# Optimization experiments

Hardware: AMD Instinct MI355X
Metric: run time of the kernel (lower is better)

## Reference

```python
import jax, jax.numpy as jnp
import numpy as np

H, C = 8, 32          # heads, channels per head; H*C = 256 triggers the LN branch
N_NODES = 30000       # nodes per node type
N_EDGES = 100000      # edges per edge type
N_TYPES = 6           # hardwired edge types (all src = Package_Name)
D_IN = 128            # raw input feature dim (Package_Name stays at 128)
LRELU_SLOPE = 0.2     # PyG GATConv default negative_slope


def _segment_softmax(e, dst, n):
    # softmax of per-edge logits e [E,H] grouped by destination node
    m = jax.ops.segment_max(e, dst, num_segments=n)
    ex = jnp.exp(e - m[dst])
    den = jax.ops.segment_sum(ex, dst, num_segments=n)
    return ex / (den[dst] + 1e-16)


def _gat(x_src, x_tgt, src, dst, Ws, Wd, a_s, a_d, b):
    # bipartite GATConv, concat heads, no self loops, no edge features
    hs = (x_src @ Ws).reshape(-1, H, C)   # [Ns,H,C]
    hd = (x_tgt @ Wd).reshape(-1, H, C)   # [Nt,H,C]
    es = jnp.einsum('nhc,hc->nh', hs, a_s)
    ed = jnp.einsum('nhc,hc->nh', hd, a_d)
    e = jax.nn.leaky_relu(es[src] + ed[dst], negative_slope=LRELU_SLOPE)  # [E,H]
    n = x_tgt.shape[0]
    alpha = _segment_softmax(e, dst, n)                                   # [E,H]
    msg = hs[src] * alpha[:, :, None]                                     # [E,H,C]
    out = jax.ops.segment_sum(msg, dst, num_segments=n).reshape(n, H * C) + b
    return out, alpha


def _ln_relu(x, g, b):
    mu = x.mean(-1, keepdims=True)
    var = ((x - mu) ** 2).mean(-1, keepdims=True)
    return jax.nn.relu((x - mu) / jnp.sqrt(var + 1e-5) * g + b)


def setup_inputs() -> dict:
    key = jax.random.key(0)
    ks = jax.random.split(key, 16)
    s = 0.05
    return {
        'x_pkg': jax.random.normal(ks[0], (N_NODES, D_IN), jnp.float32),
        'x_tgt': jax.random.normal(ks[1], (N_TYPES, N_NODES, D_IN), jnp.float32),
        'edge_index': jax.random.randint(ks[2], (N_TYPES, 2, N_EDGES), 0, N_NODES, jnp.int32),
        'W1_src': jax.random.normal(ks[3], (N_TYPES, D_IN, H * C), jnp.float32) * s,
        'W1_dst': jax.random.normal(ks[4], (N_TYPES, D_IN, H * C), jnp.float32) * s,
        'att1_src': jax.random.normal(ks[5], (N_TYPES, H, C), jnp.float32) * s,
        'att1_dst': jax.random.normal(ks[6], (N_TYPES, H, C), jnp.float32) * s,
        'b1': jnp.zeros((N_TYPES, H * C), jnp.float32),
        'W2_src': jax.random.normal(ks[7], (N_TYPES, D_IN, H * C), jnp.float32) * s,
        'W2_dst': jax.random.normal(ks[8], (N_TYPES, H * C, H * C), jnp.float32) * s,
        'att2_src': jax.random.normal(ks[9], (N_TYPES, H, C), jnp.float32) * s,
        'att2_dst': jax.random.normal(ks[10], (N_TYPES, H, C), jnp.float32) * s,
        'b2': jnp.zeros((N_TYPES, H * C), jnp.float32),
        'gamma': jnp.ones((N_TYPES, H * C), jnp.float32),
        'beta': jnp.zeros((N_TYPES, H * C), jnp.float32),
        'Wc': jax.random.normal(ks[11], (N_TYPES * H * C + D_IN, 1), jnp.float32) * s,
        'bc': jnp.zeros((1,), jnp.float32),
    }


def reference(x_pkg, x_tgt, edge_index, W1_src, W1_dst, att1_src, att1_dst, b1,
              W2_src, W2_dst, att2_src, att2_dst, b2, gamma, beta, Wc, bc):
    def layer(xt, ei, Ws, Wd, a_s, a_d, bb):
        return _gat(x_pkg, xt, ei[0], ei[1], Ws, Wd, a_s, a_d, bb)

    vlayer = jax.vmap(layer, in_axes=(0, 0, 0, 0, 0, 0, 0))

    # layer 1: Package_Name -> each of 6 target types; Package_Name itself unchanged
    out1, _ = vlayer(x_tgt, edge_index, W1_src, W1_dst, att1_src, att1_dst, b1)
    x1 = jax.vmap(_ln_relu)(out1, gamma, beta)   # module reuses ln1 after both layers

    # layer 2: src features are still the raw 128-d Package_Name features
    out2, alpha2 = vlayer(x1, edge_index, W2_src, W2_dst, att2_src, att2_dst, b2)
    x2 = jax.vmap(_ln_relu)(out2, gamma, beta)

    # global mean pool per node type, concat (6 targets then Package_Name), classify
    pooled = jnp.concatenate([x2.mean(axis=1).reshape(-1), x_pkg.mean(axis=0)])
    logits = pooled @ Wc[:, 0] + bc[0]
    return logits, alpha2
```

## Files before the change

kernel.cpp:

```cpp
#include <hip/hip_runtime.h>
#include <hip/hip_bf16.h>
#include <cstddef>

#define N_NODES 30000
#define N_EDGES 100000
#define N_TYPES 6
#define D_IN 128
#define HC 256
#define NH 8
#define CH 32

typedef __attribute__((ext_vector_type(8))) unsigned short ushort8_t;
typedef __attribute__((ext_vector_type(4))) unsigned short ushort4_t;
typedef __attribute__((ext_vector_type(8))) __bf16 bf16x8;
typedef __attribute__((ext_vector_type(4))) float floatx4;

#define L2_NPB 32
#define L2_GRID ((N_NODES + L2_NPB - 1) / L2_NPB)

__device__ inline unsigned short f2bf(float f) {
    unsigned u = __float_as_uint(f);
    u += 0x7fffu + ((u >> 16) & 1u);
    return (unsigned short)(u >> 16);
}
__device__ inline float bf2f(unsigned short u) {
    return __uint_as_float(((unsigned)u) << 16);
}

__global__ void zero4(float4* __restrict__ p, int n4) {
    int g = blockIdx.x * blockDim.x + threadIdx.x;
    if (g < n4) p[g] = make_float4(0.f, 0.f, 0.f, 0.f);
}
__global__ void zero_i(int* __restrict__ p, int n) {
    int g = blockIdx.x * blockDim.x + threadIdx.x;
    if (g < n) p[g] = 0;
}
__global__ void to_bf16(const float* __restrict__ x, unsigned short* __restrict__ o, int n4) {
    int g = blockIdx.x * blockDim.x + threadIdx.x;
    if (g >= n4) return;
    float4 v = ((const float4*)x)[g];
    ushort4_t p;
    p[0] = f2bf(v.x); p[1] = f2bf(v.y); p[2] = f2bf(v.z); p[3] = f2bf(v.w);
    *(ushort4_t*)&o[(size_t)g * 4] = p;
}

__global__ void hist_all(const int* __restrict__ ei, int* __restrict__ counts) {
    int t = blockIdx.y;
    int e = blockIdx.x * 256 + threadIdx.x;
    if (e < N_EDGES)
        atomicAdd(&counts[t * N_NODES + ei[(size_t)t * 2 * N_EDGES + N_EDGES + e]], 1);
}

#define SCAN_T 1024
#define SCAN_C 30
__global__ __launch_bounds__(1024) void scan_all(const int* __restrict__ counts_g,
                                                 int* __restrict__ row_ptr_g,
                                                 int* __restrict__ cursor_g) {
    int t = blockIdx.x;
    const int* counts = counts_g + t * N_NODES;
    int* row_ptr = row_ptr_g + t * (N_NODES + 1);
    int* cursor = cursor_g + t * N_NODES;
    __shared__ int part[SCAN_T];
    int tid = threadIdx.x;
    int base = tid * SCAN_C;
    int loc[SCAN_C];
    int s = 0;
    #pragma unroll
    for (int i = 0; i < SCAN_C; ++i) {
        int idx = base + i;
        int v = (idx < N_NODES) ? counts[idx] : 0;
        loc[i] = s; s += v;
    }
    part[tid] = s;
    __syncthreads();
    int tot = s;
    for (int d = 1; d < SCAN_T; d <<= 1) {
        int v = (tid >= d) ? part[tid - d] : 0;
        __syncthreads();
        part[tid] += v;
        __syncthreads();
    }
    int off = part[tid] - tot;
    #pragma unroll
    for (int i = 0; i < SCAN_C; ++i) {
        int idx = base + i;
        if (idx < N_NODES) { int r = off + loc[i]; row_ptr[idx] = r; cursor[idx] = r; }
    }
    if (tid == SCAN_T - 1) row_ptr[N_NODES] = part[SCAN_T - 1];
}

__global__ void fill_all(const int* __restrict__ ei, int* __restrict__ cursor,
                         int* __restrict__ elist) {
    int t = blockIdx.y;
    int e = blockIdx.x * 256 + threadIdx.x;
    if (e < N_EDGES) {
        const int* src = ei + (size_t)t * 2 * N_EDGES;
        const int* dst = src + N_EDGES;
        int pos = atomicAdd(&cursor[t * N_NODES + dst[e]], 1);
        elist[t * N_EDGES + pos] = src[e];
    }
}

__global__ void att_weight_all(const float* __restrict__ W1d, const float* __restrict__ a1d,
                               const float* __restrict__ W2d, const float* __restrict__ a2d,
                               float* __restrict__ wd1, float* __restrict__ wd2) {
    int g = blockIdx.x * blockDim.x + threadIdx.x;
    const int per_t = (D_IN + HC) * NH;
    if (g >= N_TYPES * per_t) return;
    int t = g / per_t, r = g % per_t;
    if (r < D_IN * NH) {
        int k = r >> 3, h = r & 7;
        const float* wr = W1d + (size_t)t * D_IN * HC + (size_t)k * HC + h * CH;
        const float* ar = a1d + t * HC + h * CH;
        float s = 0.f;
        #pragma unroll
        for (int c = 0; c < CH; ++c) s += wr[c] * ar[c];
        wd1[t * D_IN * NH + r] = s;
    } else {
        r -= D_IN * NH;
        int k = r >> 3, h = r & 7;
        const float* wr = W2d + (size_t)t * HC * HC + (size_t)k * HC + h * CH;
        const float* ar = a2d + t * HC + h * CH;
        float s = 0.f;
        #pragma unroll
        for (int c = 0; c < CH; ++c) s += wr[c] * ar[c];
        wd2[t * HC * NH + r] = s;
    }
}

__global__ __launch_bounds__(256) void gemm_all(const unsigned short* __restrict__ A,
                                                const float* __restrict__ W1s,
                                                const float* __restrict__ W2s,
                                                const float* __restrict__ att1,
                                                const float* __restrict__ att2,
                                                unsigned short* __restrict__ hs_all,
                                                float* __restrict__ es_all) {
    const int j = blockIdx.z;
    const float* B = (j < 6) ? W1s + (size_t)j * D_IN * HC
                             : W2s + (size_t)(j - 6) * D_IN * HC;
    const float* att = (j < 6) ? att1 + j * HC : att2 + (j - 6) * HC;
    unsigned short* Cp = hs_all + (size_t)j * N_NODES * HC;
    float* e_out = es_all + (size_t)j * N_NODES * NH;

    __shared__ unsigned short As[64 * 40];
    __shared__ unsigned short Bs[64 * 40];

    const int tid = threadIdx.x;
    const int w = tid >> 6;
    const int lane = tid & 63;
    const int col = lane & 15;
    const int quad = lane >> 4;
    const int m0 = blockIdx.x * 64;
    const int n0 = blockIdx.y * 64;

    const int am = tid >> 2;
    const int ak = (tid & 3) * 8;
    const int bk2 = (tid >> 4) * 2;
    const int bn4 = (tid & 15) * 4;

    floatx4 acc[4];
    #pragma unroll
    for (int ct = 0; ct < 4; ++ct) acc[ct] = (floatx4){0.f, 0.f, 0.f, 0.f};

    #pragma unroll
    for (int k0 = 0; k0 < D_IN; k0 += 32) {
        {
            int gm = m0 + am;
            ushort8_t v = (ushort8_t){0, 0, 0, 0, 0, 0, 0, 0};
            if (gm < N_NODES) v = *(const ushort8_t*)&A[(size_t)gm * D_IN + k0 + ak];
            *(ushort8_t*)&As[am * 40 + ak] = v;
        }
        {
            const float4 r0 = *(const float4*)&B[(size_t)(k0 + bk2) * HC + n0 + bn4];
            const float4 r1 = *(const float4*)&B[(size_t)(k0 + bk2 + 1) * HC + n0 + bn4];
            float a0[4] = {r0.x, r0.y, r0.z, r0.w};
            float a1[4] = {r1.x, r1.y, r1.z, r1.w};
            #pragma unroll
            for (int q = 0; q < 4; ++q) {
                unsigned pk = (unsigned)f2bf(a0[q]) | ((unsigned)f2bf(a1[q]) << 16);
                *(unsigned*)&Bs[(bn4 + q) * 40 + bk2] = pk;
            }
        }
        __syncthreads();
        {
            ushort8_t araw = *(const ushort8_t*)&As[(w * 16 + col) * 40 + quad * 8];
            bf16x8 af = __builtin_bit_cast(bf16x8, araw);
            #pragma unroll
            for (int ct = 0; ct < 4; ++ct) {
                ushort8_t braw = *(const ushort8_t*)&Bs[(ct * 16 + col) * 40 + quad * 8];
                bf16x8 bf = __builtin_bit_cast(bf16x8, braw);
                acc[ct] = __builtin_amdgcn_mfma_f32_16x16x32_bf16(af, bf, acc[ct], 0, 0, 0);
            }
        }
        __syncthreads();
    }

    #pragma unroll
    for (int ct = 0; ct < 4; ++ct) {
        #pragma unroll
        for (int r = 0; r < 4; ++r) {
            int gm = m0 + w * 16 + quad * 4 + r;
            if (gm < N_NODES) Cp[(size_t)gm * HC + n0 + ct * 16 + col] = f2bf(acc[ct][r]);
        }
    }

    float attv[4];
    #pragma unroll
    for (int ct = 0; ct < 4; ++ct) attv[ct] = att[n0 + ct * 16 + col];
    const int hbase = n0 >> 5;
    #pragma unroll
    for (int r = 0; r < 4; ++r) {
        float h0v = acc[0][r] * attv[0] + acc[1][r] * attv[1];
        float h1v = acc[2][r] * attv[2] + acc[3][r] * attv[3];
        #pragma unroll
        for (int off = 1; off < 16; off <<= 1) {
            h0v += __shfl_xor(h0v, off);
            h1v += __shfl_xor(h1v, off);
        }
        if (col == 0) {
            int gm = m0 + w * 16 + quad * 4 + r;
            if (gm < N_NODES) {
                e_out[gm * NH + hbase] = h0v;
                e_out[gm * NH + hbase + 1] = h1v;
            }
        }
    }
}

__global__ __launch_bounds__(256) void gather_l1_all(const int* __restrict__ row_ptr_g,
                                                     const int* __restrict__ elist_g,
                                                     const float* __restrict__ es_all,
                                                     const float* __restrict__ x_tgt,
                                                     const float* __restrict__ wd1,
                                                     const unsigned short* __restrict__ hs_all,
                                                     const float* __restrict__ b1,
                                                     const float* __restrict__ gamma,
                                                     const float* __restrict__ beta,
                                                     const float* __restrict__ wd2,
                                                     float* __restrict__ ed2g_all) {
    const int t = blockIdx.y;
    const int* row_ptr = row_ptr_g + t * (N_NODES + 1);
    const int* elist = elist_g + t * N_EDGES;
    const float* es = es_all + (size_t)t * N_NODES * NH;
    const float* xd = x_tgt + (size_t)t * N_NODES * D_IN;
    const float* w1 = wd1 + t * D_IN * NH;
    const unsigned short* hs = hs_all + (size_t)t * N_NODES * HC;
    const float* bias = b1 + t * HC;
    const float* gam = gamma + t * HC;
    const float* bet = beta + t * HC;
    const float* w2 = wd2 + t * HC * NH;
    float* ed2g = ed2g_all + (size_t)t * N_NODES * NH;

    const int lane = threadIdx.x & 63;
    const int d = blockIdx.x * 4 + (threadIdx.x >> 6);

    float e1v[8];
    #pragma unroll
    for (int h = 0; h < 8; ++h) e1v[h] = 0.f;
    #pragma unroll
    for (int rep = 0; rep < 2; ++rep) {
        int k = rep * 64 + lane;
        float xv = xd[(size_t)d * D_IN + k];
        const float* wr = w1 + k * 8;
        #pragma unroll
        for (int h = 0; h < 8; ++h) e1v[h] += xv * wr[h];
    }
    #pragma unroll
    for (int off = 1; off < 64; off <<= 1)
        #pragma unroll
        for (int h = 0; h < 8; ++h) e1v[h] += __shfl_xor(e1v[h], off);

    const int h_l = lane >> 3;
    const float ed_mine = e1v[h_l];
    const int e0 = row_ptr[d], e1n = row_ptr[d + 1];

    float den = 0.f;
    float4 acc = make_float4(0.f, 0.f, 0.f, 0.f);
    for (int i = e0; i < e1n; ++i) {
        int s = elist[i];
        float x = es[s * NH + h_l] + ed_mine;
        x = (x >= 0.f) ? x : 0.2f * x;
        float ex = __expf(x);
        den += ex;
        ushort4_t hv = *(const ushort4_t*)&hs[(size_t)s * HC + lane * 4];
        acc.x += ex * bf2f(hv[0]); acc.y += ex * bf2f(hv[1]);
        acc.z += ex * bf2f(hv[2]); acc.w += ex * bf2f(hv[3]);
    }
    float inv = 1.f / (den + 1e-16f);
    float4 bv = *(const float4*)&bias[lane * 4];
    acc.x = acc.x * inv + bv.x; acc.y = acc.y * inv + bv.y;
    acc.z = acc.z * inv + bv.z; acc.w = acc.w * inv + bv.w;

    float s1 = acc.x + acc.y + acc.z + acc.w;
    float s2 = acc.x * acc.x + acc.y * acc.y + acc.z * acc.z + acc.w * acc.w;
    #pragma unroll
    for (int off = 1; off < 64; off <<= 1) { s1 += __shfl_xor(s1, off); s2 += __shfl_xor(s2, off); }
    float mu = s1 * (1.f / 256.f);
    float var = s2 * (1.f / 256.f) - mu * mu;
    float rstd = rsqrtf(var + 1e-5f);
    float4 g4 = *(const float4*)&gam[lane * 4];
    float4 b4 = *(const float4*)&bet[lane * 4];
    float ya[4];
    ya[0] = fmaxf((acc.x - mu) * rstd * g4.x + b4.x, 0.f);
    ya[1] = fmaxf((acc.y - mu) * rstd * g4.y + b4.y, 0.f);
    ya[2] = fmaxf((acc.z - mu) * rstd * g4.z + b4.z, 0.f);
    ya[3] = fmaxf((acc.w - mu) * rstd * g4.w + b4.w, 0.f);

    float e2v[8];
    #pragma unroll
    for (int h = 0; h < 8; ++h) e2v[h] = 0.f;
    #pragma unroll
    for (int q = 0; q < 4; ++q) {
        int c = lane * 4 + q;
        const float* wr = w2 + c * 8;
        #pragma unroll
        for (int h = 0; h < 8; ++h) e2v[h] += ya[q] * wr[h];
    }
    #pragma unroll
    for (int off = 1; off < 64; off <<= 1)
        #pragma unroll
        for (int h = 0; h < 8; ++h) e2v[h] += __shfl_xor(e2v[h], off);
    if (lane < 8) ed2g[d * NH + lane] = e2v[lane];
}

__global__ __launch_bounds__(256) void gather_l2_all(const int* __restrict__ row_ptr_g,
                                                     const int* __restrict__ elist_g,
                                                     const float* __restrict__ es_all,
                                                     const float* __restrict__ ed2g_all,
                                                     const unsigned short* __restrict__ hs_all,
                                                     const float* __restrict__ b2,
                                                     const float* __restrict__ gamma,
                                                     const float* __restrict__ beta,
                                                     float* __restrict__ deng_all,
                                                     float* __restrict__ ppart) {
    const int t = blockIdx.y;
    const int* row_ptr = row_ptr_g + t * (N_NODES + 1);
    const int* elist = elist_g + t * N_EDGES;
    const float* es = es_all + (size_t)(6 + t) * N_NODES * NH;
    const float* ed2g = ed2g_all + (size_t)t * N_NODES * NH;
    const unsigned short* hs = hs_all + (size_t)(6 + t) * N_NODES * HC;
    const float* bias = b2 + t * HC;
    const float* gam = gamma + t * HC;
    const float* bet = beta + t * HC;
    float* deng = deng_all + (size_t)t * N_NODES * NH;
    float* psum_part = ppart + (size_t)t * L2_GRID * HC;

    const int tid = threadIdx.x;
    const int lane = tid & 63;
    const int w = tid >> 6;
    const int h_l = lane >> 3;
    const float4 bv = *(const float4*)&bias[lane * 4];
    const float4 g4 = *(const float4*)&gam[lane * 4];
    const float4 b4 = *(const float4*)&bet[lane * 4];

    float4 pool = make_float4(0.f, 0.f, 0.f, 0.f);
    const int base = blockIdx.x * L2_NPB;

    #pragma unroll 1
    for (int rep = 0; rep < L2_NPB / 4; ++rep) {
        const int d = base + rep * 4 + w;
        if (d >= N_NODES) break;

        const float ed_mine = ed2g[d * NH + h_l];
        const int e0 = row_ptr[d], e1n = row_ptr[d + 1];

        float den = 0.f;
        float4 acc = make_float4(0.f, 0.f, 0.f, 0.f);
        for (int i = e0; i < e1n; ++i) {
            int s = elist[i];
            float x = es[s * NH + h_l] + ed_mine;
            x = (x >= 0.f) ? x : 0.2f * x;
            float ex = __expf(x);
            den += ex;
            ushort4_t hv = *(const ushort4_t*)&hs[(size_t)s * HC + lane * 4];
            acc.x += ex * bf2f(hv[0]); acc.y += ex * bf2f(hv[1]);
            acc.z += ex * bf2f(hv[2]); acc.w += ex * bf2f(hv[3]);
        }
        if ((lane & 7) == 0) deng[d * NH + h_l] = den;
        float inv = 1.f / (den + 1e-16f);
        acc.x = acc.x * inv + bv.x; acc.y = acc.y * inv + bv.y;
        acc.z = acc.z * inv + bv.z; acc.w = acc.w * inv + bv.w;

        float s1 = acc.x + acc.y + acc.z + acc.w;
        float s2 = acc.x * acc.x + acc.y * acc.y + acc.z * acc.z + acc.w * acc.w;
        #pragma unroll
        for (int off = 1; off < 64; off <<= 1) { s1 += __shfl_xor(s1, off); s2 += __shfl_xor(s2, off); }
        float mu = s1 * (1.f / 256.f);
        float var = s2 * (1.f / 256.f) - mu * mu;
        float rstd = rsqrtf(var + 1e-5f);
        pool.x += fmaxf((acc.x - mu) * rstd * g4.x + b4.x, 0.f);
        pool.y += fmaxf((acc.y - mu) * rstd * g4.y + b4.y, 0.f);
        pool.z += fmaxf((acc.z - mu) * rstd * g4.z + b4.z, 0.f);
        pool.w += fmaxf((acc.w - mu) * rstd * g4.w + b4.w, 0.f);
    }

    __shared__ float sacc[4][260];
    *(float4*)&sacc[w][lane * 4] = pool;
    __syncthreads();
    float tot = sacc[0][tid] + sacc[1][tid] + sacc[2][tid] + sacc[3][tid];
    psum_part[(size_t)blockIdx.x * HC + tid] = tot;
}

__global__ __launch_bounds__(256) void pool_reduce_all(const float* __restrict__ ppart,
                                                       float* __restrict__ psums) {
    int t = blockIdx.y;
    const float* part = ppart + (size_t)t * L2_GRID * HC;
    int tid = threadIdx.x;
    float acc = 0.f;
    for (int b = blockIdx.x; b < L2_GRID; b += gridDim.x)
        acc += part[(size_t)b * HC + tid];
    atomicAdd(&psums[t * HC + tid], acc);
}

__global__ void alpha_all(const int* __restrict__ ei,
                          const float* __restrict__ es_all,
                          const float* __restrict__ ed2g_all,
                          const float* __restrict__ deng_all,
                          float* __restrict__ out) {
    int t = blockIdx.y;
    int g = blockIdx.x * 256 + threadIdx.x;
    if (g >= N_EDGES * NH) return;
    int e = g >> 3, h = g & 7;
    const int* src = ei + (size_t)t * 2 * N_EDGES;
    const int* dst = src + N_EDGES;
    int s = src[e], d = dst[e];
    const float* es = es_all + (size_t)(6 + t) * N_NODES * NH;
    float x = es[s * NH + h] + ed2g_all[(size_t)t * N_NODES * NH + d * NH + h];
    x = (x >= 0.f) ? x : 0.2f * x;
    out[(size_t)t * N_EDGES * NH + g] =
        __expf(x) / (deng_all[(size_t)t * N_NODES * NH + d * NH + h] + 1e-16f);
}

__global__ __launch_bounds__(256) void pkg_accum(const float* __restrict__ x, float* __restrict__ sums) {
    int tid = threadIdx.x;
    int col = tid & 127;
    int rof = tid >> 7;
    float acc = 0.f;
    for (int r = blockIdx.x * 2 + rof; r < N_NODES; r += gridDim.x * 2)
        acc += x[(size_t)r * D_IN + col];
    atomicAdd(&sums[col], acc);
}

__global__ __launch_bounds__(256) void logits_k(const float* __restrict__ psums,
                                                const float* __restrict__ ksums,
                                                const float* __restrict__ Wc,
                                                const float* __restrict__ bc,
                                                float* __restrict__ out) {
    int tid = threadIdx.x;
    const float inv = 1.f / (float)N_NODES;
    float acc = 0.f;
    for (int i = tid; i < N_TYPES * HC; i += 256) acc += psums[i] * inv * Wc[i];
    if (tid < D_IN) acc += ksums[tid] * inv * Wc[N_TYPES * HC + tid];
    #pragma unroll
    for (int off = 32; off; off >>= 1) acc += __shfl_down(acc, off);
    __shared__ float w[4];
    if ((tid & 63) == 0) w[tid >> 6] = acc;
    __syncthreads();
    if (tid == 0) out[0] = w[0] + w[1] + w[2] + w[3] + bc[0];
}

static inline void zf(float* p, int n, hipStream_t stream) {
    int n4 = (n + 3) >> 2;
    zero4<<<(n4 + 255) / 256, 256, 0, stream>>>((float4*)p, n4);
}

extern "C" void kernel_launch(void* const* d_in, const int* in_sizes, int n_in,
                              void* d_out, int out_size, void* d_ws, size_t ws_size,
                              hipStream_t stream) {
    const float* x_pkg    = (const float*)d_in[0];
    const float* x_tgt    = (const float*)d_in[1];
    const int*   ei       = (const int*)d_in[2];
    const float* W1_src   = (const float*)d_in[3];
    const float* W1_dst   = (const float*)d_in[4];
    const float* att1_src = (const float*)d_in[5];
    const float* att1_dst = (const float*)d_in[6];
    const float* b1       = (const float*)d_in[7];
    const float* W2_src   = (const float*)d_in[8];
    const float* W2_dst   = (const float*)d_in[9];
    const float* att2_src = (const float*)d_in[10];
    const float* att2_dst = (const float*)d_in[11];
    const float* b2       = (const float*)d_in[12];
    const float* gamma    = (const float*)d_in[13];
    const float* beta     = (const float*)d_in[14];
    const float* Wc       = (const float*)d_in[15];
    const float* bc       = (const float*)d_in[16];
    float* out = (float*)d_out;

    char* wsb = (char*)d_ws;
    unsigned short* xpkg_bf = (unsigned short*)wsb;
    unsigned short* hs_all  = xpkg_bf + (size_t)N_NODES * D_IN;
    float* es_all   = (float*)(hs_all + (size_t)12 * N_NODES * HC);
    float* ed2g_all = es_all + (size_t)12 * N_NODES * NH;
    float* deng_all = ed2g_all + (size_t)N_TYPES * N_NODES * NH;
    float* psums    = deng_all + (size_t)N_TYPES * N_NODES * NH;
    float* ksums    = psums + N_TYPES * HC;
    float* wd1      = ksums + D_IN;
    float* wd2      = wd1 + N_TYPES * D_IN * NH;
    float* ppart    = wd2 + N_TYPES * HC * NH;
    int* counts  = (int*)(ppart + (size_t)N_TYPES * L2_GRID * HC);
    int* row_ptr = counts + N_TYPES * N_NODES;
    int* cursor  = row_ptr + N_TYPES * (N_NODES + 1);
    int* elist   = cursor + N_TYPES * N_NODES;

    dim3 egrid((N_EDGES + 255) / 256, N_TYPES);

    zf(psums, N_TYPES * HC, stream);
    zf(ksums, D_IN, stream);
    pkg_accum<<<256, 256, 0, stream>>>(x_pkg, ksums);
    {
        int tot = N_TYPES * (D_IN + HC) * NH;
        att_weight_all<<<(tot + 255) / 256, 256, 0, stream>>>(W1_dst, att1_dst, W2_dst, att2_dst, wd1, wd2);
    }
    to_bf16<<<((N_NODES * D_IN / 4) + 255) / 256, 256, 0, stream>>>(x_pkg, xpkg_bf, N_NODES * D_IN / 4);
    zero_i<<<(N_TYPES * N_NODES + 255) / 256, 256, 0, stream>>>(counts, N_TYPES * N_NODES);
    hist_all<<<egrid, 256, 0, stream>>>(ei, counts);
    scan_all<<<N_TYPES, SCAN_T, 0, stream>>>(counts, row_ptr, cursor);
    fill_all<<<egrid, 256, 0, stream>>>(ei, cursor, elist);

    {
        dim3 g((N_NODES + 63) / 64, HC / 64, 12);
        gemm_all<<<g, 256, 0, stream>>>(xpkg_bf, W1_src, W2_src, att1_src, att2_src,
                                        hs_all, es_all);
    }

    {
        dim3 g(N_NODES / 4, N_TYPES);
        gather_l1_all<<<g, 256, 0, stream>>>(row_ptr, elist, es_all, x_tgt, wd1, hs_all,
                                             b1, gamma, beta, wd2, ed2g_all);
    }

    {
        dim3 g(L2_GRID, N_TYPES);
        gather_l2_all<<<g, 256, 0, stream>>>(row_ptr, elist, es_all, ed2g_all, hs_all,
                                             b2, gamma, beta, deng_all, ppart);
    }
    {
        dim3 g(8, N_TYPES);
        pool_reduce_all<<<g, 256, 0, stream>>>(ppart, psums);
    }
    {
        dim3 g((N_EDGES * NH + 255) / 256, N_TYPES);
        alpha_all<<<g, 256, 0, stream>>>(ei, es_all, ed2g_all, deng_all, out + 1);
    }

    logits_k<<<1, 256, 0, stream>>>(psums, ksums, Wc, bc, out);
}
```

Baseline: 843.0 us.

## Batch edge gathers four-wide with prefetched indices and hoist layer-1 dst logits

Each wave now loads up to 64 source indices at once and passes them around with shuffles. It then processes edges four at a time, so several independent hs/es loads are in flight together. The layer-1 destination attention logits move into a separate ed1_all kernel over a transposed wd1 layout, and the layer-2 logit projection now goes through swizzled shared memory instead of full-wave shuffle reductions. L2_NPB is halved to give more blocks. Costs are one extra kernel launch, an extra ed1 buffer round trip, and masked redundant loads on edge tails.

```diff
diff --git a/kernel.cpp b/kernel.cpp
--- a/kernel.cpp
+++ b/kernel.cpp
@@ -15,7 +15,7 @@
 typedef __attribute__((ext_vector_type(8))) __bf16 bf16x8;
 typedef __attribute__((ext_vector_type(4))) float floatx4;
 
-#define L2_NPB 32
+#define L2_NPB 16
 #define L2_GRID ((N_NODES + L2_NPB - 1) / L2_NPB)
 
 __device__ inline unsigned short f2bf(float f) {
@@ -115,7 +115,7 @@
         float s = 0.f;
         #pragma unroll
         for (int c = 0; c < CH; ++c) s += wr[c] * ar[c];
-        wd1[t * D_IN * NH + r] = s;
+        wd1[t * D_IN * NH + h * D_IN + k] = s;
     } else {
         r -= D_IN * NH;
         int k = r >> 3, h = r & 7;
@@ -124,8 +124,29 @@
         float s = 0.f;
         #pragma unroll
         for (int c = 0; c < CH; ++c) s += wr[c] * ar[c];
-        wd2[t * HC * NH + r] = s;
-    }
+        wd2[t * HC * NH + h * HC + k] = s;
+    }
+}
+
+__global__ __launch_bounds__(256) void ed1_all(const float* __restrict__ x_tgt,
+                                               const float* __restrict__ wd1,
+                                               float* __restrict__ ed1g) {
+    const int t = blockIdx.y;
+    const int lane = threadIdx.x & 63;
+    const int wv = threadIdx.x >> 6;
+    const int n8 = lane >> 3, h = lane & 7;
+    const int node = blockIdx.x * 32 + wv * 8 + n8;
+    if (node >= N_NODES) return;
+    const float* xr = x_tgt + ((size_t)t * N_NODES + node) * D_IN;
+    const float* wp = wd1 + t * D_IN * NH + h * D_IN;
+    float acc = 0.f;
+    #pragma unroll
+    for (int k = 0; k < D_IN; k += 4) {
+        const float4 x4 = *(const float4*)&xr[k];
+        const float4 w4 = *(const float4*)&wp[k];
+        acc += x4.x * w4.x + x4.y * w4.y + x4.z * w4.z + x4.w * w4.w;
+    }
+    ed1g[((size_t)t * N_NODES + node) * NH + h] = acc;
 }
 
 __global__ __launch_bounds__(256) void gemm_all(const unsigned short* __restrict__ A,
@@ -227,11 +248,58 @@
     }
 }
 
+__device__ inline void edge4(const float* __restrict__ es,
+                             const unsigned short* __restrict__ hs,
+                             int s_pre, int i, int cm,
+                             int h_l, int lane, float ed_mine,
+                             float& den, float4& acc) {
+    const int i1 = (i + 1 < cm) ? i + 1 : cm;
+    const int i2 = (i + 2 < cm) ? i + 2 : cm;
+    const int i3 = (i + 3 < cm) ? i + 3 : cm;
+    const int s0 = __shfl(s_pre, i);
+    const int s1 = __shfl(s_pre, i1);
+    const int s2 = __shfl(s_pre, i2);
+    const int s3 = __shfl(s_pre, i3);
+    float q0 = es[s0 * NH + h_l];
+    float q1 = es[s1 * NH + h_l];
+    float q2 = es[s2 * NH + h_l];
+    float q3 = es[s3 * NH + h_l];
+    const ushort4_t v0 = *(const ushort4_t*)&hs[(size_t)s0 * HC + lane * 4];
+    const ushort4_t v1 = *(const ushort4_t*)&hs[(size_t)s1 * HC + lane * 4];
+    const ushort4_t v2 = *(const ushort4_t*)&hs[(size_t)s2 * HC + lane * 4];
+    const ushort4_t v3 = *(const ushort4_t*)&hs[(size_t)s3 * HC + lane * 4];
+    q0 += ed_mine; q0 = (q0 >= 0.f) ? q0 : 0.2f * q0;
+    q1 += ed_mine; q1 = (q1 >= 0.f) ? q1 : 0.2f * q1;
+    q2 += ed_mine; q2 = (q2 >= 0.f) ? q2 : 0.2f * q2;
+    q3 += ed_mine; q3 = (q3 >= 0.f) ? q3 : 0.2f * q3;
+    const float x0 = __expf(q0);
+    const float x1 = (i + 1 <= cm) ? __expf(q1) : 0.f;
+    const float x2 = (i + 2 <= cm) ? __expf(q2) : 0.f;
+    const float x3 = (i + 3 <= cm) ? __expf(q3) : 0.f;
+    den += (x0 + x1) + (x2 + x3);
+    acc.x += x0 * bf2f(v0[0]) + x1 * bf2f(v1[0]) + x2 * bf2f(v2[0]) + x3 * bf2f(v3[0]);
+    acc.y += x0 * bf2f(v0[1]) + x1 * bf2f(v1[1]) + x2 * bf2f(v2[1]) + x3 * bf2f(v3[1]);
+    acc.z += x0 * bf2f(v0[2]) + x1 * bf2f(v1[2]) + x2 * bf2f(v2[2]) + x3 * bf2f(v3[2]);
+    acc.w += x0 * bf2f(v0[3]) + x1 * bf2f(v1[3]) + x2 * bf2f(v2[3]) + x3 * bf2f(v3[3]);
+}
+
+__device__ inline void edge1(const float* __restrict__ es,
+                             const unsigned short* __restrict__ hs,
+                             int s, int h_l, int lane, float ed_mine,
+                             float& den, float4& acc) {
+    float x = es[s * NH + h_l] + ed_mine;
+    x = (x >= 0.f) ? x : 0.2f * x;
+    const float ex = __expf(x);
+    den += ex;
+    const ushort4_t hv = *(const ushort4_t*)&hs[(size_t)s * HC + lane * 4];
+    acc.x += ex * bf2f(hv[0]); acc.y += ex * bf2f(hv[1]);
+    acc.z += ex * bf2f(hv[2]); acc.w += ex * bf2f(hv[3]);
+}
+
 __global__ __launch_bounds__(256) void gather_l1_all(const int* __restrict__ row_ptr_g,
                                                      const int* __restrict__ elist_g,
                                                      const float* __restrict__ es_all,
-                                                     const float* __restrict__ x_tgt,
-                                                     const float* __restrict__ wd1,
+                                                     const float* __restrict__ ed1g,
                                                      const unsigned short* __restrict__ hs_all,
                                                      const float* __restrict__ b1,
                                                      const float* __restrict__ gamma,
@@ -242,8 +310,6 @@
     const int* row_ptr = row_ptr_g + t * (N_NODES + 1);
     const int* elist = elist_g + t * N_EDGES;
     const float* es = es_all + (size_t)t * N_NODES * NH;
-    const float* xd = x_tgt + (size_t)t * N_NODES * D_IN;
-    const float* w1 = wd1 + t * D_IN * NH;
     const unsigned short* hs = hs_all + (size_t)t * N_NODES * HC;
     const float* bias = b1 + t * HC;
     const float* gam = gamma + t * HC;
@@ -252,42 +318,30 @@
     float* ed2g = ed2g_all + (size_t)t * N_NODES * NH;
 
     const int lane = threadIdx.x & 63;
-    const int d = blockIdx.x * 4 + (threadIdx.x >> 6);
-
-    float e1v[8];
-    #pragma unroll
-    for (int h = 0; h < 8; ++h) e1v[h] = 0.f;
-    #pragma unroll
-    for (int rep = 0; rep < 2; ++rep) {
-        int k = rep * 64 + lane;
-        float xv = xd[(size_t)d * D_IN + k];
-        const float* wr = w1 + k * 8;
-        #pragma unroll
-        for (int h = 0; h < 8; ++h) e1v[h] += xv * wr[h];
-    }
-    #pragma unroll
-    for (int off = 1; off < 64; off <<= 1)
-        #pragma unroll
-        for (int h = 0; h < 8; ++h) e1v[h] += __shfl_xor(e1v[h], off);
-
+    const int w = threadIdx.x >> 6;
+    const int d = blockIdx.x * 4 + w;
     const int h_l = lane >> 3;
-    const float ed_mine = e1v[h_l];
+
+    const float ed_mine = ed1g[((size_t)t * N_NODES + d) * NH + h_l];
     const int e0 = row_ptr[d], e1n = row_ptr[d + 1];
+    const int cnt = e1n - e0;
+    int s_pre = 0;
+    if (lane < cnt) s_pre = elist[e0 + lane];
 
     float den = 0.f;
     float4 acc = make_float4(0.f, 0.f, 0.f, 0.f);
-    for (int i = e0; i < e1n; ++i) {
-        int s = elist[i];
-        float x = es[s * NH + h_l] + ed_mine;
-        x = (x >= 0.f) ? x : 0.2f * x;
-        float ex = __expf(x);
-        den += ex;
-        ushort4_t hv = *(const ushort4_t*)&hs[(size_t)s * HC + lane * 4];
-        acc.x += ex * bf2f(hv[0]); acc.y += ex * bf2f(hv[1]);
-        acc.z += ex * bf2f(hv[2]); acc.w += ex * bf2f(hv[3]);
-    }
-    float inv = 1.f / (den + 1e-16f);
-    float4 bv = *(const float4*)&bias[lane * 4];
+    if (cnt > 0) {
+        const int c1 = (cnt < 64) ? cnt : 64;
+        const int cm = c1 - 1;
+        for (int i = 0; i < c1; i += 4)
+            edge4(es, hs, s_pre, i, cm, h_l, lane, ed_mine, den, acc);
+        if (cnt > 64)
+            for (int ii = e0 + 64; ii < e1n; ++ii)
+                edge1(es, hs, elist[ii], h_l, lane, ed_mine, den, acc);
+    }
+
+    const float inv = 1.f / (den + 1e-16f);
+    const float4 bv = *(const float4*)&bias[lane * 4];
     acc.x = acc.x * inv + bv.x; acc.y = acc.y * inv + bv.y;
     acc.z = acc.z * inv + bv.z; acc.w = acc.w * inv + bv.w;
 
@@ -295,32 +349,37 @@
     float s2 = acc.x * acc.x + acc.y * acc.y + acc.z * acc.z + acc.w * acc.w;
     #pragma unroll
     for (int off = 1; off < 64; off <<= 1) { s1 += __shfl_xor(s1, off); s2 += __shfl_xor(s2, off); }
-    float mu = s1 * (1.f / 256.f);
-    float var = s2 * (1.f / 256.f) - mu * mu;
-    float rstd = rsqrtf(var + 1e-5f);
-    float4 g4 = *(const float4*)&gam[lane * 4];
-    float4 b4 = *(const float4*)&bet[lane * 4];
-    float ya[4];
-    ya[0] = fmaxf((acc.x - mu) * rstd * g4.x + b4.x, 0.f);
-    ya[1] = fmaxf((acc.y - mu) * rstd * g4.y + b4.y, 0.f);
-    ya[2] = fmaxf((acc.z - mu) * rstd * g4.z + b4.z, 0.f);
-    ya[3] = fmaxf((acc.w - mu) * rstd * g4.w + b4.w, 0.f);
-
-    float e2v[8];
-    #pragma unroll
-    for (int h = 0; h < 8; ++h) e2v[h] = 0.f;
-    #pragma unroll
-    for (int q = 0; q < 4; ++q) {
-        int c = lane * 4 + q;
-        const float* wr = w2 + c * 8;
-        #pragma unroll
-        for (int h = 0; h < 8; ++h) e2v[h] += ya[q] * wr[h];
-    }
-    #pragma unroll
-    for (int off = 1; off < 64; off <<= 1)
-        #pragma unroll
-        for (int h = 0; h < 8; ++h) e2v[h] += __shfl_xor(e2v[h], off);
-    if (lane < 8) ed2g[d * NH + lane] = e2v[lane];
+    const float mu = s1 * (1.f / 256.f);
+    const float var = s2 * (1.f / 256.f) - mu * mu;
+    const float rstd = rsqrtf(var + 1e-5f);
+    const float4 g4 = *(const float4*)&gam[lane * 4];
+    const float4 b4 = *(const float4*)&bet[lane * 4];
+    const float ya0 = fmaxf((acc.x - mu) * rstd * g4.x + b4.x, 0.f);
+    const float ya1 = fmaxf((acc.y - mu) * rstd * g4.y + b4.y, 0.f);
+    const float ya2 = fmaxf((acc.z - mu) * rstd * g4.z + b4.z, 0.f);
+    const float ya3 = fmaxf((acc.w - mu) * rstd * g4.w + b4.w, 0.f);
+
+    __shared__ __align__(16) float ya_s[4][256];
+    {
+        const int c0 = lane * 4;
+        const int widx = (c0 & ~31) | ((c0 & 31) ^ ((lane >> 3) << 2));
+        *(float4*)&ya_s[w][widx] = make_float4(ya0, ya1, ya2, ya3);
+    }
+    const int k8 = lane >> 3;
+    const int h = lane & 7;
+    const float* w2h = w2 + h * HC;
+    float e2 = 0.f;
+    #pragma unroll
+    for (int jj = 0; jj < 8; ++jj) {
+        const int idx = k8 * 32 + ((jj * 4) ^ (k8 << 2));
+        const float4 y = *(const float4*)&ya_s[w][idx];
+        const float4 wv = *(const float4*)&w2h[k8 * 32 + jj * 4];
+        e2 += y.x * wv.x + y.y * wv.y + y.z * wv.z + y.w * wv.w;
+    }
+    e2 += __shfl_xor(e2, 8);
+    e2 += __shfl_xor(e2, 16);
+    e2 += __shfl_xor(e2, 32);
+    if (lane < 8) ed2g[d * NH + lane] = e2;
 }
 
 __global__ __launch_bounds__(256) void gather_l2_all(const int* __restrict__ row_ptr_g,
@@ -363,21 +422,23 @@
 
         const float ed_mine = ed2g[d * NH + h_l];
         const int e0 = row_ptr[d], e1n = row_ptr[d + 1];
+        const int cnt = e1n - e0;
+        int s_pre = 0;
+        if (lane < cnt) s_pre = elist[e0 + lane];
 
         float den = 0.f;
         float4 acc = make_float4(0.f, 0.f, 0.f, 0.f);
-        for (int i = e0; i < e1n; ++i) {
-            int s = elist[i];
-            float x = es[s * NH + h_l] + ed_mine;
-            x = (x >= 0.f) ? x : 0.2f * x;
-            float ex = __expf(x);
-            den += ex;
-            ushort4_t hv = *(const ushort4_t*)&hs[(size_t)s * HC + lane * 4];
-            acc.x += ex * bf2f(hv[0]); acc.y += ex * bf2f(hv[1]);
-            acc.z += ex * bf2f(hv[2]); acc.w += ex * bf2f(hv[3]);
+        if (cnt > 0) {
+            const int c1 = (cnt < 64) ? cnt : 64;
+            const int cm = c1 - 1;
+            for (int i = 0; i < c1; i += 4)
+                edge4(es, hs, s_pre, i, cm, h_l, lane, ed_mine, den, acc);
+            if (cnt > 64)
+                for (int ii = e0 + 64; ii < e1n; ++ii)
+                    edge1(es, hs, elist[ii], h_l, lane, ed_mine, den, acc);
         }
         if ((lane & 7) == 0) deng[d * NH + h_l] = den;
-        float inv = 1.f / (den + 1e-16f);
+        const float inv = 1.f / (den + 1e-16f);
         acc.x = acc.x * inv + bv.x; acc.y = acc.y * inv + bv.y;
         acc.z = acc.z * inv + bv.z; acc.w = acc.w * inv + bv.w;
 
@@ -385,16 +446,16 @@
         float s2 = acc.x * acc.x + acc.y * acc.y + acc.z * acc.z + acc.w * acc.w;
         #pragma unroll
         for (int off = 1; off < 64; off <<= 1) { s1 += __shfl_xor(s1, off); s2 += __shfl_xor(s2, off); }
-        float mu = s1 * (1.f / 256.f);
-        float var = s2 * (1.f / 256.f) - mu * mu;
-        float rstd = rsqrtf(var + 1e-5f);
+        const float mu = s1 * (1.f / 256.f);
+        const float var = s2 * (1.f / 256.f) - mu * mu;
+        const float rstd = rsqrtf(var + 1e-5f);
         pool.x += fmaxf((acc.x - mu) * rstd * g4.x + b4.x, 0.f);
         pool.y += fmaxf((acc.y - mu) * rstd * g4.y + b4.y, 0.f);
         pool.z += fmaxf((acc.z - mu) * rstd * g4.z + b4.z, 0.f);
         pool.w += fmaxf((acc.w - mu) * rstd * g4.w + b4.w, 0.f);
     }
 
-    __shared__ float sacc[4][260];
+    __shared__ __align__(16) float sacc[4][260];
     *(float4*)&sacc[w][lane * 4] = pool;
     __syncthreads();
     float tot = sacc[0][tid] + sacc[1][tid] + sacc[2][tid] + sacc[3][tid];
@@ -496,7 +557,8 @@
     float* ksums    = psums + N_TYPES * HC;
     float* wd1      = ksums + D_IN;
     float* wd2      = wd1 + N_TYPES * D_IN * NH;
-    float* ppart    = wd2 + N_TYPES * HC * NH;
+    float* ed1g     = wd2 + N_TYPES * HC * NH;
+    float* ppart    = ed1g + (size_t)N_TYPES * N_NODES * NH;
     int* counts  = (int*)(ppart + (size_t)N_TYPES * L2_GRID * HC);
     int* row_ptr = counts + N_TYPES * N_NODES;
     int* cursor  = row_ptr + N_TYPES * (N_NODES + 1);
@@ -510,6 +572,10 @@
     {
         int tot = N_TYPES * (D_IN + HC) * NH;
         att_weight_all<<<(tot + 255) / 256, 256, 0, stream>>>(W1_dst, att1_dst, W2_dst, att2_dst, wd1, wd2);
+    }
+    {
+        dim3 g((N_NODES + 31) / 32, N_TYPES);
+        ed1_all<<<g, 256, 0, stream>>>(x_tgt, wd1, ed1g);
     }
     to_bf16<<<((N_NODES * D_IN / 4) + 255) / 256, 256, 0, stream>>>(x_pkg, xpkg_bf, N_NODES * D_IN / 4);
     zero_i<<<(N_TYPES * N_NODES + 255) / 256, 256, 0, stream>>>(counts, N_TYPES * N_NODES);
@@ -525,7 +591,7 @@
 
     {
         dim3 g(N_NODES / 4, N_TYPES);
-        gather_l1_all<<<g, 256, 0, stream>>>(row_ptr, elist, es_all, x_tgt, wd1, hs_all,
+        gather_l1_all<<<g, 256, 0, stream>>>(row_ptr, elist, es_all, ed1g, hs_all,
                                              b1, gamma, beta, wd2, ed2g_all);
     }
 
```

Measured after the change: 880.2 us. 1.04x slower.
